# Kernel tuning notes

Measured on AMD Instinct MI355X. Metric: run time of the kernel, lower is better.

The kernel has to match this reference:

```python
import jax, jax.numpy as jnp
import numpy as np

PATTERN = np.array([3, 5, 8, 12, 16, 21, 27, 36], dtype=np.int64)
REPEATS = 32
GROUPS = np.tile(PATTERN, REPEATS)   # 256 ragged group sizes
G = int(GROUPS.size)                 # 256 groups
F = int(GROUPS.sum())                # 4096 total features
B = 8192
SPLIT = G - 3                        # split_idx = num_groups - 3
H1, H2 = 512, 256
EPS = 1e-5


def _xavier(key, shape):
    fan_in, fan_out = shape
    lim = float(np.sqrt(6.0 / (fan_in + fan_out)))
    return jax.random.uniform(key, shape, jnp.float32, -lim, lim)


def setup_inputs() -> dict:
    key = jax.random.key(0)
    ks = jax.random.split(key, 8)
    # segment id for every feature column -> its gene group
    seg = jnp.asarray(np.repeat(np.arange(G), GROUPS), dtype=jnp.int32)
    x = jax.random.normal(ks[0], (B, F), jnp.float32)
    # per-group Linear(group,1) weights, flattened; xavier limit per group size
    lims = np.sqrt(6.0 / (GROUPS + 1.0))
    w_gene = jax.random.uniform(ks[1], (F,), jnp.float32, -1.0, 1.0) * jnp.asarray(np.repeat(lims, GROUPS), jnp.float32)
    return {
        "x": x, "seg": seg,
        "w_gene": w_gene, "b_gene": jnp.zeros((G,), jnp.float32),
        "W1g1": _xavier(ks[2], (SPLIT, H1)), "b1g1": jnp.zeros((H1,), jnp.float32),
        "W2g1": _xavier(ks[3], (H1, H2)), "b2g1": jnp.zeros((H2,), jnp.float32),
        "W1g2": _xavier(ks[4], (3, H1)), "b1g2": jnp.zeros((H1,), jnp.float32),
        "W2g2": _xavier(ks[5], (H1, H2)), "b2g2": jnp.zeros((H2,), jnp.float32),
        "gamma1g1": jnp.ones((H1,), jnp.float32), "beta1g1": jnp.zeros((H1,), jnp.float32),
        "gamma2g1": jnp.ones((H2,), jnp.float32), "beta2g1": jnp.zeros((H2,), jnp.float32),
        "gamma1g2": jnp.ones((H1,), jnp.float32), "beta1g2": jnp.zeros((H1,), jnp.float32),
        "gamma2g2": jnp.ones((H2,), jnp.float32), "beta2g2": jnp.zeros((H2,), jnp.float32),
        "W_out": _xavier(ks[6], (2 * H2, 1)), "b_out": jnp.zeros((1,), jnp.float32),
        "W_res": _xavier(ks[7], (G, 1)), "b_res": jnp.zeros((1,), jnp.float32),
    }


def _bn(h, gamma, beta):
    # BatchNorm1d in training mode: biased batch statistics over the batch axis
    mu = jnp.mean(h, axis=0)
    var = jnp.var(h, axis=0)
    return (h - mu) * jax.lax.rsqrt(var + EPS) * gamma + beta


def reference(x, seg, w_gene, b_gene, W1g1, b1g1, W2g1, b2g1, W1g2, b1g2, W2g2, b2g2,
              gamma1g1, beta1g1, gamma2g1, beta2g1, gamma1g2, beta1g2, gamma2g2, beta2g2,
              W_out, b_out, W_res, b_res):
    # The loop of tiny Linear(group,1)+ReLU over contiguous feature slices is
    # exactly a ragged weighted segment-sum: [B, F] -> [B, G]
    gene = jax.nn.relu(jax.ops.segment_sum((x * w_gene).T, seg, num_segments=G).T + b_gene)
    g1, g2 = gene[:, :SPLIT], gene[:, SPLIT:]
    # dropout p = 0.0 -> identity
    h1 = jax.nn.relu(_bn(g1 @ W1g1 + b1g1, gamma1g1, beta1g1))
    h1 = jax.nn.relu(_bn(h1 @ W2g1 + b2g1, gamma2g1, beta2g1))
    h2 = jax.nn.relu(_bn(g2 @ W1g2 + b1g2, gamma1g2, beta1g2))
    h2 = jax.nn.relu(_bn(h2 @ W2g2 + b2g2, gamma2g2, beta2g2))
    combined = jnp.concatenate([h1, h2], axis=1)           # [B, 2*H2]
    return combined @ W_out + b_out + gene @ W_res + b_res  # [B, 1]
```

## Files before the change

kernel.cpp:

```cpp
#include <hip/hip_runtime.h>
#include <cstddef>

#define BATCH  8192
#define NFEAT  4096
#define NGRP   256
#define NSPLIT 253
#define NH1    512
#define NH2    256
#define EPSV   1e-5f

typedef __bf16 bf16_8 __attribute__((ext_vector_type(8)));
typedef float  f32x4  __attribute__((ext_vector_type(4)));

__constant__ int c_prefix[8] = {0,3,8,16,28,44,65,92};
__constant__ int c_gsize[8]  = {3,5,8,12,16,21,27,36};

__global__ __launch_bounds__(256) void gene_kernel(const float* __restrict__ x,
        const float* __restrict__ wg, const float* __restrict__ bg,
        float* __restrict__ gene, __bf16* __restrict__ geneb)
{
    __shared__ float prod[NFEAT];
    int t = threadIdx.x;
    size_t row = blockIdx.x;
    const float4* xv = (const float4*)(x + row * NFEAT);
    const float4* wv = (const float4*)wg;
    float4* pv = (float4*)prod;
#pragma unroll
    for (int i = 0; i < 4; i++) {
        int idx = t + 256 * i;
        float4 a = xv[idx], w = wv[idx];
        float4 p; p.x = a.x*w.x; p.y = a.y*w.y; p.z = a.z*w.z; p.w = a.w*w.w;
        pv[idx] = p;
    }
    __syncthreads();
    int g = t;
    int start = (g >> 3) * 128 + c_prefix[g & 7];
    int len = c_gsize[g & 7];
    float s = 0.f;
    for (int i = 0; i < len; i++) s += prod[start + i];
    s += bg[g];
    s = fmaxf(s, 0.f);
    gene[row * NGRP + g] = s;
    geneb[row * NGRP + g] = (__bf16)s;
}

__global__ __launch_bounds__(256) void transposeW(const float* __restrict__ src,
        __bf16* __restrict__ dst, int K, int N, int Kp)
{
    __shared__ float tile[32][33];
    int kt = blockIdx.x * 32, nt = blockIdx.y * 32;
    int tx = threadIdx.x & 31, ty = threadIdx.x >> 5;
    for (int r = ty; r < 32; r += 8) {
        int k = kt + r, n = nt + tx;
        tile[r][tx] = (k < K && n < N) ? src[(size_t)k * N + n] : 0.f;
    }
    __syncthreads();
    for (int r = ty; r < 32; r += 8) {
        int n = nt + r, k = kt + tx;
        if (n < N && k < Kp) dst[(size_t)n * Kp + k] = (__bf16)tile[tx][r];
    }
}

__global__ __launch_bounds__(256) void gemm_bf16(
    const __bf16* __restrict__ A, int lda, int K,
    const __bf16* __restrict__ WT, int n_total,
    const float* __restrict__ bias,
    __bf16* __restrict__ C,
    float* __restrict__ csum, float* __restrict__ csq,
    const float* __restrict__ a_sum, const float* __restrict__ a_sq,
    const float* __restrict__ a_gamma, const float* __restrict__ a_beta)
{
    __shared__ __align__(16) __bf16 As[64][72];
    __shared__ __align__(16) __bf16 Bs[64][72];
    __shared__ float bnsc[512];
    __shared__ float bnsh[512];
    __shared__ float sred[64];
    __shared__ float qred[64];

    int t = threadIdx.x;
    int n0 = blockIdx.x * 64;
    int m0 = blockIdx.y * 64;
    bool bn = (a_sum != nullptr);
    if (bn) {
        const float invB = 1.f / (float)BATCH;
        for (int k = t; k < K; k += 256) {
            float mu  = a_sum[k] * invB;
            float var = a_sq[k] * invB - mu * mu;
            float sc  = a_gamma[k] * rsqrtf(var + EPSV);
            bnsc[k] = sc;
            bnsh[k] = a_beta[k] - mu * sc;
        }
    }
    if (t < 64) { sred[t] = 0.f; qred[t] = 0.f; }

    int lane = t & 63, w = t >> 6;
    int wm = (w & 1) * 32, wn = (w >> 1) * 32;
    int fm = lane & 15, quad = lane >> 4;

    f32x4 acc[2][2];
#pragma unroll
    for (int i = 0; i < 2; i++)
#pragma unroll
        for (int j = 0; j < 2; j++) acc[i][j] = (f32x4){0.f, 0.f, 0.f, 0.f};

    int r0 = t >> 3;
    int kc = (t & 7) * 8;

    int nk = K >> 6;
    for (int kt = 0; kt < nk; kt++) {
        int kk = kt << 6;
        __syncthreads();
#pragma unroll
        for (int h = 0; h < 2; h++) {
            int row = r0 + h * 32;
            uint4 raw = *(const uint4*)(A + (size_t)(m0 + row) * lda + kk + kc);
            if (bn) {
                __bf16 vals[8];
#pragma unroll
                for (int c = 0; c < 4; c++) {
                    unsigned uu = (&raw.x)[c];
                    int kg = kk + kc + 2 * c;
                    float flo = __uint_as_float(uu << 16);
                    float fhi = __uint_as_float(uu & 0xffff0000u);
                    flo = fmaxf(fmaf(flo, bnsc[kg],     bnsh[kg]),     0.f);
                    fhi = fmaxf(fmaf(fhi, bnsc[kg + 1], bnsh[kg + 1]), 0.f);
                    vals[2 * c]     = (__bf16)flo;
                    vals[2 * c + 1] = (__bf16)fhi;
                }
                *(bf16_8*)&As[row][kc] = *(bf16_8*)vals;
            } else {
                *(uint4*)&As[row][kc] = raw;
            }
        }
#pragma unroll
        for (int h = 0; h < 2; h++) {
            int row = r0 + h * 32;
            *(uint4*)&Bs[row][kc] = *(const uint4*)(WT + (size_t)(n0 + row) * K + kk + kc);
        }
        __syncthreads();
#pragma unroll
        for (int kc2 = 0; kc2 < 64; kc2 += 32) {
            bf16_8 a0 = *(const bf16_8*)&As[wm + fm][kc2 + quad * 8];
            bf16_8 a1 = *(const bf16_8*)&As[wm + 16 + fm][kc2 + quad * 8];
            bf16_8 b0 = *(const bf16_8*)&Bs[wn + fm][kc2 + quad * 8];
            bf16_8 b1 = *(const bf16_8*)&Bs[wn + 16 + fm][kc2 + quad * 8];
            acc[0][0] = __builtin_amdgcn_mfma_f32_16x16x32_bf16(a0, b0, acc[0][0], 0, 0, 0);
            acc[0][1] = __builtin_amdgcn_mfma_f32_16x16x32_bf16(a0, b1, acc[0][1], 0, 0, 0);
            acc[1][0] = __builtin_amdgcn_mfma_f32_16x16x32_bf16(a1, b0, acc[1][0], 0, 0, 0);
            acc[1][1] = __builtin_amdgcn_mfma_f32_16x16x32_bf16(a1, b1, acc[1][1], 0, 0, 0);
        }
    }

    float myS[2] = {0.f, 0.f}, myQ[2] = {0.f, 0.f};
#pragma unroll
    for (int j = 0; j < 2; j++) {
        int col = n0 + wn + j * 16 + fm;
        float bv = bias[col];
#pragma unroll
        for (int i = 0; i < 2; i++) {
#pragma unroll
            for (int r = 0; r < 4; r++) {
                float v = acc[i][j][r] + bv;
                int row = m0 + wm + i * 16 + quad * 4 + r;
                C[(size_t)row * n_total + col] = (__bf16)v;
                myS[j] += v;
                myQ[j] += v * v;
            }
        }
    }
#pragma unroll
    for (int j = 0; j < 2; j++) {
        atomicAdd(&sred[wn + j * 16 + fm], myS[j]);
        atomicAdd(&qred[wn + j * 16 + fm], myQ[j]);
    }
    __syncthreads();
    if (t < 64) {
        atomicAdd(&csum[n0 + t], sred[t]);
        atomicAdd(&csq[n0 + t], qred[t]);
    }
}

__global__ __launch_bounds__(256) void b2l1_kernel(const float* __restrict__ gene,
    const float* __restrict__ W, const float* __restrict__ bias,
    __bf16* __restrict__ out, float* __restrict__ csum, float* __restrict__ csq)
{
    __shared__ float Ws[3 * 512];
    __shared__ float bsh[512];
    __shared__ float gv[16][3];
    int t = threadIdx.x;
    for (int i = t; i < 1536; i += 256) Ws[i] = W[i];
    for (int i = t; i < 512; i += 256) bsh[i] = bias[i];
    int row0 = blockIdx.x * 16;
    if (t < 48) gv[t / 3][t % 3] = gene[(size_t)(row0 + t / 3) * NGRP + NSPLIT + (t % 3)];
    __syncthreads();
    int c0 = t, c1 = t + 256;
    float s0 = 0, q0 = 0, s1 = 0, q1 = 0;
    for (int r = 0; r < 16; r++) {
        float a = gv[r][0], b = gv[r][1], c = gv[r][2];
        float v0 = bsh[c0] + a * Ws[c0] + b * Ws[512 + c0] + c * Ws[1024 + c0];
        float v1 = bsh[c1] + a * Ws[c1] + b * Ws[512 + c1] + c * Ws[1024 + c1];
        size_t base = (size_t)(row0 + r) * NH1;
        out[base + c0] = (__bf16)v0; out[base + c1] = (__bf16)v1;
        s0 += v0; q0 += v0 * v0; s1 += v1; q1 += v1 * v1;
    }
    atomicAdd(&csum[c0], s0); atomicAdd(&csq[c0], q0);
    atomicAdd(&csum[c1], s1); atomicAdd(&csq[c1], q1);
}

__global__ __launch_bounds__(256) void final_kernel(
    const __bf16* __restrict__ h1, const __bf16* __restrict__ h2,
    const float* __restrict__ gene,
    const float* __restrict__ s1, const float* __restrict__ q1,
    const float* __restrict__ gm1, const float* __restrict__ bt1,
    const float* __restrict__ s2, const float* __restrict__ q2,
    const float* __restrict__ gm2, const float* __restrict__ bt2,
    const float* __restrict__ Wout, const float* __restrict__ bo,
    const float* __restrict__ Wres, const float* __restrict__ br,
    float* __restrict__ outp)
{
    int t = threadIdx.x, lane = t & 63, wv = t >> 6;
    int row = blockIdx.x * 4 + wv;
    const float invB = 1.f / (float)BATCH;
    float acc = 0.f;
#pragma unroll
    for (int ii = 0; ii < 4; ii++) {
        int c = lane + ii * 64;
        float mu  = s1[c] * invB;
        float var = q1[c] * invB - mu * mu;
        float sc  = gm1[c] * rsqrtf(var + EPSV);
        float v   = ((float)h1[(size_t)row * NH2 + c] - mu) * sc + bt1[c];
        acc += fmaxf(v, 0.f) * Wout[c];
        mu  = s2[c] * invB;
        var = q2[c] * invB - mu * mu;
        sc  = gm2[c] * rsqrtf(var + EPSV);
        v   = ((float)h2[(size_t)row * NH2 + c] - mu) * sc + bt2[c];
        acc += fmaxf(v, 0.f) * Wout[NH2 + c];
        acc += gene[(size_t)row * NGRP + c] * Wres[c];
    }
#pragma unroll
    for (int off = 32; off > 0; off >>= 1) acc += __shfl_down(acc, off, 64);
    if (lane == 0) outp[row] = acc + bo[0] + br[0];
}

extern "C" void kernel_launch(void* const* d_in, const int* in_sizes, int n_in,
                              void* d_out, int out_size, void* d_ws, size_t ws_size,
                              hipStream_t stream)
{
    (void)in_sizes; (void)n_in; (void)out_size; (void)ws_size;
    const float* x        = (const float*)d_in[0];
    const float* wgene    = (const float*)d_in[2];
    const float* bgene    = (const float*)d_in[3];
    const float* W1g1     = (const float*)d_in[4];
    const float* b1g1     = (const float*)d_in[5];
    const float* W2g1     = (const float*)d_in[6];
    const float* b2g1     = (const float*)d_in[7];
    const float* W1g2     = (const float*)d_in[8];
    const float* b1g2     = (const float*)d_in[9];
    const float* W2g2     = (const float*)d_in[10];
    const float* b2g2     = (const float*)d_in[11];
    const float* gamma1g1 = (const float*)d_in[12];
    const float* beta1g1  = (const float*)d_in[13];
    const float* gamma2g1 = (const float*)d_in[14];
    const float* beta2g1  = (const float*)d_in[15];
    const float* gamma1g2 = (const float*)d_in[16];
    const float* beta1g2  = (const float*)d_in[17];
    const float* gamma2g2 = (const float*)d_in[18];
    const float* beta2g2  = (const float*)d_in[19];
    const float* Wout     = (const float*)d_in[20];
    const float* bout     = (const float*)d_in[21];
    const float* Wres     = (const float*)d_in[22];
    const float* bres     = (const float*)d_in[23];
    float* outp = (float*)d_out;

    char* p = (char*)d_ws;
    float*  gene  = (float*)p;            p += (size_t)BATCH * NGRP * 4;
    __bf16* geneb = (__bf16*)p;           p += (size_t)BATCH * NGRP * 2;
    __bf16* h1pre = (__bf16*)p;           p += (size_t)BATCH * NH1 * 2;
    __bf16* bufA  = (__bf16*)p;           p += (size_t)BATCH * NH1 * 2;
    __bf16* h1b   = (__bf16*)p;           p += (size_t)BATCH * NH2 * 2;
    __bf16* h2b   = (__bf16*)p;           p += (size_t)BATCH * NH2 * 2;
    __bf16* w1t   = (__bf16*)p;           p += (size_t)NH1 * 256 * 2;
    __bf16* w2at  = (__bf16*)p;           p += (size_t)NH2 * NH1 * 2;
    __bf16* w2bt  = (__bf16*)p;           p += (size_t)NH2 * NH1 * 2;
    float*  st    = (float*)p;
    float* s1a = st;          float* q1a = st + 512;
    float* s1b = st + 1024;   float* q1b = st + 1536;
    float* s2a = st + 2048;   float* q2a = st + 2560;
    float* s2b = st + 3072;   float* q2b = st + 3584;

    hipMemsetAsync(st, 0, 4096 * sizeof(float), stream);

    transposeW<<<dim3(256 / 32, NH1 / 32), 256, 0, stream>>>(W1g1, w1t, NSPLIT, NH1, 256);
    transposeW<<<dim3(NH1 / 32, NH2 / 32), 256, 0, stream>>>(W2g1, w2at, NH1, NH2, NH1);
    transposeW<<<dim3(NH1 / 32, NH2 / 32), 256, 0, stream>>>(W2g2, w2bt, NH1, NH2, NH1);

    gene_kernel<<<BATCH, 256, 0, stream>>>(x, wgene, bgene, gene, geneb);

    gemm_bf16<<<dim3(NH1 / 64, BATCH / 64), 256, 0, stream>>>(
        geneb, NGRP, 256, w1t, NH1, b1g1, h1pre, s1a, q1a,
        nullptr, nullptr, nullptr, nullptr);

    b2l1_kernel<<<BATCH / 16, 256, 0, stream>>>(gene, W1g2, b1g2, bufA, s2a, q2a);

    gemm_bf16<<<dim3(NH2 / 64, BATCH / 64), 256, 0, stream>>>(
        h1pre, NH1, NH1, w2at, NH2, b2g1, h1b, s1b, q1b,
        s1a, q1a, gamma1g1, beta1g1);

    gemm_bf16<<<dim3(NH2 / 64, BATCH / 64), 256, 0, stream>>>(
        bufA, NH1, NH1, w2bt, NH2, b2g2, h2b, s2b, q2b,
        s2a, q2a, gamma1g2, beta1g2);

    final_kernel<<<BATCH / 4, 256, 0, stream>>>(
        h1b, h2b, gene,
        s1b, q1b, gamma2g1, beta2g1,
        s2b, q2b, gamma2g2, beta2g2,
        Wout, bout, Wres, bres, outp);
}
```

Baseline: 322.4 us.

## Parallelize gene segment-sum, merge branch GEMMs, vectorize final kernel

The gene kernel now pads shared memory to avoid bank conflicts and splits each group's sum across 8 lanes with a shuffle reduction, replacing one thread walking up to 36 elements. The two second-layer GEMMs become a single launch using blockIdx.z, and the first GEMM drops its BN-prologue branch. The small-branch layer kernel handles 64 rows per block instead of 16. The final kernel switches to float4 and ushort4 vectorized loads. Together these aim to cut launch count, per-thread serial work and scalar memory traffic.

```diff
diff --git a/kernel.cpp b/kernel.cpp
--- a/kernel.cpp
+++ b/kernel.cpp
@@ -19,29 +19,40 @@
         const float* __restrict__ wg, const float* __restrict__ bg,
         float* __restrict__ gene, __bf16* __restrict__ geneb)
 {
-    __shared__ float prod[NFEAT];
+    __shared__ float prod[NFEAT + 32 * 8];
+    __shared__ float gout[NGRP];
     int t = threadIdx.x;
     size_t row = blockIdx.x;
     const float4* xv = (const float4*)(x + row * NFEAT);
     const float4* wv = (const float4*)wg;
-    float4* pv = (float4*)prod;
 #pragma unroll
     for (int i = 0; i < 4; i++) {
         int idx = t + 256 * i;
         float4 a = xv[idx], w = wv[idx];
         float4 p; p.x = a.x*w.x; p.y = a.y*w.y; p.z = a.z*w.z; p.w = a.w*w.w;
-        pv[idx] = p;
-    }
-    __syncthreads();
-    int g = t;
-    int start = (g >> 3) * 128 + c_prefix[g & 7];
-    int len = c_gsize[g & 7];
-    float s = 0.f;
-    for (int i = 0; i < len; i++) s += prod[start + i];
-    s += bg[g];
-    s = fmaxf(s, 0.f);
-    gene[row * NGRP + g] = s;
-    geneb[row * NGRP + g] = (__bf16)s;
+        int f = idx * 4;
+        *(float4*)&prod[f + ((f >> 7) << 3)] = p;
+    }
+    __syncthreads();
+    int sub = t & 7, gidx = t >> 3;
+    int gi  = gidx & 7, fbo = gidx >> 3;
+    int pre = c_prefix[gi], len = c_gsize[gi];
+#pragma unroll
+    for (int s = 0; s < 8; s++) {
+        int base = (4 * s + fbo) * 136 + pre;
+        float v = 0.f;
+        for (int j = sub; j < len; j += 8) v += prod[base + j];
+        v += __shfl_down(v, 4, 8);
+        v += __shfl_down(v, 2, 8);
+        v += __shfl_down(v, 1, 8);
+        if (sub == 0) gout[(s << 5) + gidx] = v;
+    }
+    __syncthreads();
+    {
+        float s = fmaxf(gout[t] + bg[t], 0.f);
+        gene[row * NGRP + t]  = s;
+        geneb[row * NGRP + t] = (__bf16)s;
+    }
 }
 
 __global__ __launch_bounds__(256) void transposeW(const float* __restrict__ src,
@@ -66,31 +77,16 @@
     const __bf16* __restrict__ WT, int n_total,
     const float* __restrict__ bias,
     __bf16* __restrict__ C,
-    float* __restrict__ csum, float* __restrict__ csq,
-    const float* __restrict__ a_sum, const float* __restrict__ a_sq,
-    const float* __restrict__ a_gamma, const float* __restrict__ a_beta)
+    float* __restrict__ csum, float* __restrict__ csq)
 {
     __shared__ __align__(16) __bf16 As[64][72];
     __shared__ __align__(16) __bf16 Bs[64][72];
-    __shared__ float bnsc[512];
-    __shared__ float bnsh[512];
     __shared__ float sred[64];
     __shared__ float qred[64];
 
     int t = threadIdx.x;
     int n0 = blockIdx.x * 64;
     int m0 = blockIdx.y * 64;
-    bool bn = (a_sum != nullptr);
-    if (bn) {
-        const float invB = 1.f / (float)BATCH;
-        for (int k = t; k < K; k += 256) {
-            float mu  = a_sum[k] * invB;
-            float var = a_sq[k] * invB - mu * mu;
-            float sc  = a_gamma[k] * rsqrtf(var + EPSV);
-            bnsc[k] = sc;
-            bnsh[k] = a_beta[k] - mu * sc;
-        }
-    }
     if (t < 64) { sred[t] = 0.f; qred[t] = 0.f; }
 
     int lane = t & 63, w = t >> 6;
@@ -113,28 +109,7 @@
 #pragma unroll
         for (int h = 0; h < 2; h++) {
             int row = r0 + h * 32;
-            uint4 raw = *(const uint4*)(A + (size_t)(m0 + row) * lda + kk + kc);
-            if (bn) {
-                __bf16 vals[8];
-#pragma unroll
-                for (int c = 0; c < 4; c++) {
-                    unsigned uu = (&raw.x)[c];
-                    int kg = kk + kc + 2 * c;
-                    float flo = __uint_as_float(uu << 16);
-                    float fhi = __uint_as_float(uu & 0xffff0000u);
-                    flo = fmaxf(fmaf(flo, bnsc[kg],     bnsh[kg]),     0.f);
-                    fhi = fmaxf(fmaf(fhi, bnsc[kg + 1], bnsh[kg + 1]), 0.f);
-                    vals[2 * c]     = (__bf16)flo;
-                    vals[2 * c + 1] = (__bf16)fhi;
-                }
-                *(bf16_8*)&As[row][kc] = *(bf16_8*)vals;
-            } else {
-                *(uint4*)&As[row][kc] = raw;
-            }
-        }
-#pragma unroll
-        for (int h = 0; h < 2; h++) {
-            int row = r0 + h * 32;
+            *(uint4*)&As[row][kc] = *(const uint4*)(A + (size_t)(m0 + row) * lda + kk + kc);
             *(uint4*)&Bs[row][kc] = *(const uint4*)(WT + (size_t)(n0 + row) * K + kk + kc);
         }
         __syncthreads();
@@ -157,16 +132,14 @@
         int col = n0 + wn + j * 16 + fm;
         float bv = bias[col];
 #pragma unroll
-        for (int i = 0; i < 2; i++) {
+        for (int i = 0; i < 2; i++)
 #pragma unroll
             for (int r = 0; r < 4; r++) {
                 float v = acc[i][j][r] + bv;
                 int row = m0 + wm + i * 16 + quad * 4 + r;
                 C[(size_t)row * n_total + col] = (__bf16)v;
-                myS[j] += v;
-                myQ[j] += v * v;
+                myS[j] += v; myQ[j] += v * v;
             }
-        }
     }
 #pragma unroll
     for (int j = 0; j < 2; j++) {
@@ -180,22 +153,142 @@
     }
 }
 
+__global__ __launch_bounds__(256) void gemm2_dual(
+    const __bf16* A0, const __bf16* A1,
+    const __bf16* WT0, const __bf16* WT1,
+    const float* bias0, const float* bias1,
+    __bf16* C0, __bf16* C1,
+    float* csum0, float* csq0, float* csum1, float* csq1,
+    const float* as0, const float* aq0, const float* ag0, const float* ab0,
+    const float* as1, const float* aq1, const float* ag1, const float* ab1)
+{
+    const int K = NH1, n_total = NH2;
+    __shared__ __align__(16) __bf16 As[64][72];
+    __shared__ __align__(16) __bf16 Bs[64][72];
+    __shared__ float bnsc[NH1];
+    __shared__ float bnsh[NH1];
+    __shared__ float sred[64];
+    __shared__ float qred[64];
+
+    int z = blockIdx.z;
+    const __bf16* A    = z ? A1 : A0;
+    const __bf16* WT   = z ? WT1 : WT0;
+    const float*  bias = z ? bias1 : bias0;
+    __bf16*       C    = z ? C1 : C0;
+    float* csum = z ? csum1 : csum0;
+    float* csq  = z ? csq1  : csq0;
+    const float* a_sum = z ? as1 : as0;
+    const float* a_sq  = z ? aq1 : aq0;
+    const float* a_g   = z ? ag1 : ag0;
+    const float* a_b   = z ? ab1 : ab0;
+
+    int t = threadIdx.x;
+    int n0 = blockIdx.x * 64;
+    int m0 = blockIdx.y * 64;
+    {
+        const float invB = 1.f / (float)BATCH;
+        for (int k = t; k < K; k += 256) {
+            float mu  = a_sum[k] * invB;
+            float var = a_sq[k] * invB - mu * mu;
+            float sc  = a_g[k] * rsqrtf(var + EPSV);
+            bnsc[k] = sc;
+            bnsh[k] = a_b[k] - mu * sc;
+        }
+    }
+    if (t < 64) { sred[t] = 0.f; qred[t] = 0.f; }
+
+    int lane = t & 63, w = t >> 6;
+    int wm = (w & 1) * 32, wn = (w >> 1) * 32;
+    int fm = lane & 15, quad = lane >> 4;
+
+    f32x4 acc[2][2];
+#pragma unroll
+    for (int i = 0; i < 2; i++)
+#pragma unroll
+        for (int j = 0; j < 2; j++) acc[i][j] = (f32x4){0.f, 0.f, 0.f, 0.f};
+
+    int r0 = t >> 3;
+    int kc = (t & 7) * 8;
+
+    for (int kt = 0; kt < (K >> 6); kt++) {
+        int kk = kt << 6;
+        __syncthreads();
+#pragma unroll
+        for (int h = 0; h < 2; h++) {
+            int row = r0 + h * 32;
+            uint4 raw = *(const uint4*)(A + (size_t)(m0 + row) * K + kk + kc);
+            __bf16 vals[8];
+#pragma unroll
+            for (int c = 0; c < 4; c++) {
+                unsigned uu = (&raw.x)[c];
+                int kg = kk + kc + 2 * c;
+                float flo = __uint_as_float(uu << 16);
+                float fhi = __uint_as_float(uu & 0xffff0000u);
+                flo = fmaxf(fmaf(flo, bnsc[kg],     bnsh[kg]),     0.f);
+                fhi = fmaxf(fmaf(fhi, bnsc[kg + 1], bnsh[kg + 1]), 0.f);
+                vals[2 * c]     = (__bf16)flo;
+                vals[2 * c + 1] = (__bf16)fhi;
+            }
+            *(bf16_8*)&As[row][kc] = *(bf16_8*)vals;
+            *(uint4*)&Bs[row][kc] = *(const uint4*)(WT + (size_t)(n0 + row) * K + kk + kc);
+        }
+        __syncthreads();
+#pragma unroll
+        for (int kc2 = 0; kc2 < 64; kc2 += 32) {
+            bf16_8 a0 = *(const bf16_8*)&As[wm + fm][kc2 + quad * 8];
+            bf16_8 a1 = *(const bf16_8*)&As[wm + 16 + fm][kc2 + quad * 8];
+            bf16_8 b0 = *(const bf16_8*)&Bs[wn + fm][kc2 + quad * 8];
+            bf16_8 b1 = *(const bf16_8*)&Bs[wn + 16 + fm][kc2 + quad * 8];
+            acc[0][0] = __builtin_amdgcn_mfma_f32_16x16x32_bf16(a0, b0, acc[0][0], 0, 0, 0);
+            acc[0][1] = __builtin_amdgcn_mfma_f32_16x16x32_bf16(a0, b1, acc[0][1], 0, 0, 0);
+            acc[1][0] = __builtin_amdgcn_mfma_f32_16x16x32_bf16(a1, b0, acc[1][0], 0, 0, 0);
+            acc[1][1] = __builtin_amdgcn_mfma_f32_16x16x32_bf16(a1, b1, acc[1][1], 0, 0, 0);
+        }
+    }
+
+    float myS[2] = {0.f, 0.f}, myQ[2] = {0.f, 0.f};
+#pragma unroll
+    for (int j = 0; j < 2; j++) {
+        int col = n0 + wn + j * 16 + fm;
+        float bv = bias[col];
+#pragma unroll
+        for (int i = 0; i < 2; i++)
+#pragma unroll
+            for (int r = 0; r < 4; r++) {
+                float v = acc[i][j][r] + bv;
+                int row = m0 + wm + i * 16 + quad * 4 + r;
+                C[(size_t)row * n_total + col] = (__bf16)v;
+                myS[j] += v; myQ[j] += v * v;
+            }
+    }
+#pragma unroll
+    for (int j = 0; j < 2; j++) {
+        atomicAdd(&sred[wn + j * 16 + fm], myS[j]);
+        atomicAdd(&qred[wn + j * 16 + fm], myQ[j]);
+    }
+    __syncthreads();
+    if (t < 64) {
+        atomicAdd(&csum[n0 + t], sred[t]);
+        atomicAdd(&csq[n0 + t], qred[t]);
+    }
+}
+
 __global__ __launch_bounds__(256) void b2l1_kernel(const float* __restrict__ gene,
     const float* __restrict__ W, const float* __restrict__ bias,
     __bf16* __restrict__ out, float* __restrict__ csum, float* __restrict__ csq)
 {
     __shared__ float Ws[3 * 512];
     __shared__ float bsh[512];
-    __shared__ float gv[16][3];
+    __shared__ float gv[64][3];
     int t = threadIdx.x;
     for (int i = t; i < 1536; i += 256) Ws[i] = W[i];
     for (int i = t; i < 512; i += 256) bsh[i] = bias[i];
-    int row0 = blockIdx.x * 16;
-    if (t < 48) gv[t / 3][t % 3] = gene[(size_t)(row0 + t / 3) * NGRP + NSPLIT + (t % 3)];
+    int row0 = blockIdx.x * 64;
+    if (t < 192) gv[t / 3][t % 3] = gene[(size_t)(row0 + t / 3) * NGRP + NSPLIT + (t % 3)];
     __syncthreads();
     int c0 = t, c1 = t + 256;
     float s0 = 0, q0 = 0, s1 = 0, q1 = 0;
-    for (int r = 0; r < 16; r++) {
+    for (int r = 0; r < 64; r++) {
         float a = gv[r][0], b = gv[r][1], c = gv[r][2];
         float v0 = bsh[c0] + a * Ws[c0] + b * Ws[512 + c0] + c * Ws[1024 + c0];
         float v1 = bsh[c1] + a * Ws[c1] + b * Ws[512 + c1] + c * Ws[1024 + c1];
@@ -220,22 +313,32 @@
 {
     int t = threadIdx.x, lane = t & 63, wv = t >> 6;
     int row = blockIdx.x * 4 + wv;
+    int c = lane * 4;
     const float invB = 1.f / (float)BATCH;
+    float4 vs1 = *(const float4*)&s1[c],  vq1 = *(const float4*)&q1[c];
+    float4 vg1 = *(const float4*)&gm1[c], vb1 = *(const float4*)&bt1[c];
+    float4 vs2 = *(const float4*)&s2[c],  vq2 = *(const float4*)&q2[c];
+    float4 vg2 = *(const float4*)&gm2[c], vb2 = *(const float4*)&bt2[c];
+    float4 wo1 = *(const float4*)&Wout[c];
+    float4 wo2 = *(const float4*)&Wout[NH2 + c];
+    float4 wr  = *(const float4*)&Wres[c];
+    ushort4 u1 = *(const ushort4*)((const unsigned short*)h1 + (size_t)row * NH2 + c);
+    ushort4 u2 = *(const ushort4*)((const unsigned short*)h2 + (size_t)row * NH2 + c);
+    float4 gv  = *(const float4*)&gene[(size_t)row * NGRP + c];
     float acc = 0.f;
 #pragma unroll
-    for (int ii = 0; ii < 4; ii++) {
-        int c = lane + ii * 64;
-        float mu  = s1[c] * invB;
-        float var = q1[c] * invB - mu * mu;
-        float sc  = gm1[c] * rsqrtf(var + EPSV);
-        float v   = ((float)h1[(size_t)row * NH2 + c] - mu) * sc + bt1[c];
-        acc += fmaxf(v, 0.f) * Wout[c];
-        mu  = s2[c] * invB;
-        var = q2[c] * invB - mu * mu;
-        sc  = gm2[c] * rsqrtf(var + EPSV);
-        v   = ((float)h2[(size_t)row * NH2 + c] - mu) * sc + bt2[c];
-        acc += fmaxf(v, 0.f) * Wout[NH2 + c];
-        acc += gene[(size_t)row * NGRP + c] * Wres[c];
+    for (int e = 0; e < 4; e++) {
+        float h1f = __uint_as_float((unsigned)(&u1.x)[e] << 16);
+        float h2f = __uint_as_float((unsigned)(&u2.x)[e] << 16);
+        float mu  = (&vs1.x)[e] * invB;
+        float var = (&vq1.x)[e] * invB - mu * mu;
+        float v   = (h1f - mu) * (&vg1.x)[e] * rsqrtf(var + EPSV) + (&vb1.x)[e];
+        acc += fmaxf(v, 0.f) * (&wo1.x)[e];
+        mu  = (&vs2.x)[e] * invB;
+        var = (&vq2.x)[e] * invB - mu * mu;
+        v   = (h2f - mu) * (&vg2.x)[e] * rsqrtf(var + EPSV) + (&vb2.x)[e];
+        acc += fmaxf(v, 0.f) * (&wo2.x)[e];
+        acc += (&gv.x)[e] * (&wr.x)[e];
     }
 #pragma unroll
     for (int off = 32; off > 0; off >>= 1) acc += __shfl_down(acc, off, 64);
@@ -297,17 +400,14 @@
     gene_kernel<<<BATCH, 256, 0, stream>>>(x, wgene, bgene, gene, geneb);
 
     gemm_bf16<<<dim3(NH1 / 64, BATCH / 64), 256, 0, stream>>>(
-        geneb, NGRP, 256, w1t, NH1, b1g1, h1pre, s1a, q1a,
-        nullptr, nullptr, nullptr, nullptr);
-
-    b2l1_kernel<<<BATCH / 16, 256, 0, stream>>>(gene, W1g2, b1g2, bufA, s2a, q2a);
-
-    gemm_bf16<<<dim3(NH2 / 64, BATCH / 64), 256, 0, stream>>>(
-        h1pre, NH1, NH1, w2at, NH2, b2g1, h1b, s1b, q1b,
-        s1a, q1a, gamma1g1, beta1g1);
-
-    gemm_bf16<<<dim3(NH2 / 64, BATCH / 64), 256, 0, stream>>>(
-        bufA, NH1, NH1, w2bt, NH2, b2g2, h2b, s2b, q2b,
+        geneb, NGRP, 256, w1t, NH1, b1g1, h1pre, s1a, q1a);
+
+    b2l1_kernel<<<BATCH / 64, 256, 0, stream>>>(gene, W1g2, b1g2, bufA, s2a, q2a);
+
+    gemm2_dual<<<dim3(NH2 / 64, BATCH / 64, 2), 256, 0, stream>>>(
+        h1pre, bufA, w2at, w2bt, b2g1, b2g2, h1b, h2b,
+        s1b, q1b, s2b, q2b,
+        s1a, q1a, gamma1g1, beta1g1,
         s2a, q2a, gamma1g2, beta1g2);
 
     final_kernel<<<BATCH / 4, 256, 0, stream>>>(
```

Result: faster. 299.9 us (-7.0%).
